# Performance work log

Hardware: AMD Instinct MI355X
Metric: run time of the kernel (lower is better)

## Reference

```python
import jax, jax.numpy as jnp
import numpy as np

RMS_EPS = 1e-8
Q_EPS = 1e-5

def rms_norm(x):
    # RMSNorm without learnable scale, as in BitNet reference BitLinear
    return x * jax.lax.rsqrt(jnp.mean(x * x, axis=-1, keepdims=True) + RMS_EPS)

def activation_quant(x):
    # per-token absmax int8 quant/dequant
    scale = 127.0 / jnp.clip(jnp.max(jnp.abs(x), axis=-1, keepdims=True), Q_EPS)
    return jnp.clip(jnp.round(x * scale), -128, 127) / scale

def weight_quant(w):
    # ternary absmean quant/dequant
    scale = 1.0 / jnp.clip(jnp.mean(jnp.abs(w)), Q_EPS)
    return jnp.clip(jnp.round(w * scale), -1, 1) / scale

def bitlinear(x, w):
    # forward path of BitLinear: RMSNorm -> quantized matmul (STE is identity in fwd)
    xn = rms_norm(x)
    xq = xn + jax.lax.stop_gradient(activation_quant(xn) - xn)
    wq = w + jax.lax.stop_gradient(weight_quant(w) - w)
    return jnp.einsum('bsh,oh->bso', xq, wq)

def setup_inputs() -> dict:
    key = jax.random.key(0)
    k1, k2, k3 = jax.random.split(key, 3)
    H, I = 2048, 8192  # hidden_size, intermediate_size = 4*H
    x = jax.random.normal(k1, (4, 2048, H), jnp.float32)
    w_gate = jax.random.normal(k2, (2 * I, H), jnp.float32) * 0.02
    w_down = jax.random.normal(k3, (H, I), jnp.float32) * 0.02
    return {"x": x, "w_gate": w_gate, "w_down": w_down}

def reference(x, w_gate, w_down):
    y = bitlinear(x, w_gate)          # [B,S,2I]
    gate, v = jnp.split(y, 2, axis=-1)
    return bitlinear(jax.nn.silu(gate) * v, w_down)  # [B,S,H]
```

## Files before the change

kernel.cpp:

```cpp
#include <hip/hip_runtime.h>


using char8  = __attribute__((ext_vector_type(8))) signed char;
using int4v  = __attribute__((ext_vector_type(4))) int;
using half8  = __attribute__((ext_vector_type(8))) _Float16;

__device__ __forceinline__ void glds16(const void* g, void* l) {
  __builtin_amdgcn_global_load_lds((const __attribute__((address_space(1))) void*)g,
                                   (__attribute__((address_space(3))) void*)l, 16, 0, 0);
}

#define SB0() __builtin_amdgcn_sched_barrier(0)

__global__ __launch_bounds__(256) void reduce_abs_kernel(
    const float4* __restrict__ w, float* __restrict__ partials, int n4) {
  int t = threadIdx.x;
  int gid = blockIdx.x * 256 + t;
  int stride = gridDim.x * 256;
  float s = 0.f;
  for (int i = gid; i < n4; i += stride) {
    float4 u = w[i];
    s += fabsf(u.x) + fabsf(u.y) + fabsf(u.z) + fabsf(u.w);
  }
  __shared__ float sm[256];
  sm[t] = s; __syncthreads();
  for (int off = 128; off > 0; off >>= 1) {
    if (t < off) sm[t] += sm[t + off];
    __syncthreads();
  }
  if (t == 0) partials[blockIdx.x] = sm[0];
}

__global__ __launch_bounds__(256) void finalize_kernel(
    const float* __restrict__ pf, float* __restrict__ scales) {
  __shared__ float sm[256];
  int t = threadIdx.x;
  float s = pf[t] + pf[t + 256] + pf[t + 512] + pf[t + 768];
  sm[t] = s; __syncthreads();
  for (int off = 128; off > 0; off >>= 1) {
    if (t < off) sm[t] += sm[t + off];
    __syncthreads();
  }
  if (t == 0) {
    float c = fmaxf(sm[0] / 33554432.0f, 1e-5f);
    scales[0] = c; scales[2] = 1.0f / c;
  }
  __syncthreads();
  s = pf[1024 + t] + pf[1280 + t] + pf[1536 + t] + pf[1792 + t];
  sm[t] = s; __syncthreads();
  for (int off = 128; off > 0; off >>= 1) {
    if (t < off) sm[t] += sm[t + off];
    __syncthreads();
  }
  if (t == 0) {
    float c = fmaxf(sm[0] / 16777216.0f, 1e-5f);
    scales[1] = c; scales[3] = 1.0f / c;
  }
}

__global__ __launch_bounds__(256) void quant_weight_kernel(
    const float4* __restrict__ w, char8* __restrict__ wq,
    const float* __restrict__ invp, int n8) {
  float inv = *invp;
  int stride = gridDim.x * 256;
  for (int i = blockIdx.x * 256 + threadIdx.x; i < n8; i += stride) {
    float4 a = w[2 * i], b = w[2 * i + 1];
    float v[8] = {a.x, a.y, a.z, a.w, b.x, b.y, b.z, b.w};
    char8 o;
#pragma unroll
    for (int j = 0; j < 8; ++j) {
      float q = rintf(v[j] * inv);
      q = fminf(fmaxf(q, -1.f), 1.f);
      o[j] = (signed char)(int)q;
    }
    wq[i] = o;
  }
}

__global__ __launch_bounds__(256) void act_quant_f32_kernel(
    const float* __restrict__ in, signed char* __restrict__ out,
    float* __restrict__ fscale) {
  const int token = blockIdx.x, t = threadIdx.x;
  const float4* row = (const float4*)(in + (size_t)token * 2048);
  float4 a = row[2 * t], b = row[2 * t + 1];
  float v[8] = {a.x, a.y, a.z, a.w, b.x, b.y, b.z, b.w};
  float ss = 0.f, am = 0.f;
#pragma unroll
  for (int j = 0; j < 8; ++j) { ss += v[j] * v[j]; am = fmaxf(am, fabsf(v[j])); }
  __shared__ float s1[256], s2[256];
  s1[t] = ss; s2[t] = am; __syncthreads();
  for (int off = 128; off > 0; off >>= 1) {
    if (t < off) { s1[t] += s1[t + off]; s2[t] = fmaxf(s2[t], s2[t + off]); }
    __syncthreads();
  }
  float r = 1.0f / sqrtf(s1[0] * (1.0f / 2048.0f) + 1e-8f);
  float f = fmaxf(s2[0] * r, 1e-5f);
  float s = 127.0f / f;
  if (t == 0) fscale[token] = f * (1.0f / 127.0f);
  char8 o;
#pragma unroll
  for (int j = 0; j < 8; ++j) {
    float q = rintf((v[j] * r) * s);
    q = fminf(fmaxf(q, -128.f), 127.f);
    o[j] = (signed char)(int)q;
  }
  ((char8*)(out + (size_t)token * 2048))[t] = o;
}

__global__ __launch_bounds__(256) void act_quant_h_kernel(
    const _Float16* __restrict__ in, signed char* __restrict__ out,
    float* __restrict__ fscale) {
  const int token = blockIdx.x, t = threadIdx.x;
  const half8* row = (const half8*)(in + (size_t)token * 8192);
  float v[32];
  float ss = 0.f, am = 0.f;
#pragma unroll
  for (int c = 0; c < 4; ++c) {
    half8 u = row[c * 256 + t];
#pragma unroll
    for (int j = 0; j < 8; ++j) {
      float f = (float)u[j]; v[c * 8 + j] = f;
      ss += f * f; am = fmaxf(am, fabsf(f));
    }
  }
  __shared__ float s1[256], s2[256];
  s1[t] = ss; s2[t] = am; __syncthreads();
  for (int off = 128; off > 0; off >>= 1) {
    if (t < off) { s1[t] += s1[t + off]; s2[t] = fmaxf(s2[t], s2[t + off]); }
    __syncthreads();
  }
  float r = 1.0f / sqrtf(s1[0] * (1.0f / 8192.0f) + 1e-8f);
  float f = fmaxf(s2[0] * r, 1e-5f);
  float s = 127.0f / f;
  if (t == 0) fscale[token] = f * (1.0f / 127.0f);
#pragma unroll
  for (int c = 0; c < 4; ++c) {
    char8 o;
#pragma unroll
    for (int j = 0; j < 8; ++j) {
      float q = rintf((v[c * 8 + j] * r) * s);
      q = fminf(fmaxf(q, -128.f), 127.f);
      o[j] = (signed char)(int)q;
    }
    ((char8*)(out + (size_t)token * 8192))[c * 256 + t] = o;
  }
}

__global__ __launch_bounds__(256, 2) void gemm1_kernel(
    const signed char* __restrict__ A,
    const signed char* __restrict__ B,
    const float* __restrict__ f1, const float* __restrict__ cgp,
    _Float16* __restrict__ Z) {
  constexpr int K = 2048, I = 8192, NT = K / 64;
  constexpr int BUF = 24576;
  __shared__ __align__(16) signed char Ls[3 * BUF];
  const int t0 = blockIdx.y * 128, n0 = blockIdx.x * 128;
  const int tid = threadIdx.x, w = tid >> 6, l = tid & 63;
  const int wm = (w >> 1) * 64, wn = (w & 1) * 64;
  const int lrow = l & 15, lchunk = (l >> 4) * 16;

  int4v ag[4][4], av[4][4];
#pragma unroll
  for (int i = 0; i < 4; ++i)
#pragma unroll
    for (int j = 0; j < 4; ++j) { ag[i][j] = {0,0,0,0}; av[i][j] = {0,0,0,0}; }

  const signed char* src[6];
  int dst[6];
#pragma unroll
  for (int r = 0; r < 6; ++r) {
    int u = w * 6 + r;
    if (u < 8) {
      src[r] = A + (size_t)(t0 + u * 16 + lrow) * K + lchunk;
      dst[r] = u * 1024;
    } else {
      int v = u - 8;
      int grow = (v < 8) ? (n0 + v * 16 + lrow) : (I + n0 + (v - 8) * 16 + lrow);
      src[r] = B + (size_t)grow * K + lchunk;
      dst[r] = 8192 + v * 1024;
    }
  }

#pragma unroll
  for (int p = 0; p < 2; ++p)
#pragma unroll
    for (int r = 0; r < 6; ++r) glds16(src[r] + p * 64, &Ls[p * BUF + dst[r]]);
  asm volatile("s_waitcnt vmcnt(6)" ::: "memory");
  __builtin_amdgcn_s_barrier();
  SB0();

  const int aoff = (wm >> 4) * 1024 + l * 16;
  const int goff = 8192 + (wn >> 4) * 1024 + l * 16;
  const int voff = goff + 8 * 1024;

  int curo = 0;
  for (int it = 0; it < NT; ++it) {
    int stgo = curo + 2 * BUF; if (stgo >= 3 * BUF) stgo -= 3 * BUF;
    const bool stg = (it + 2 < NT);
    const int ko = (it + 2) * 64;
    int4v af[4], bg[4], bv[4];

#pragma unroll
    for (int j = 0; j < 4; ++j) {
      if (j == 0) {
#pragma unroll
        for (int i = 0; i < 4; ++i) af[i] = *(const int4v*)&Ls[curo + aoff + i * 1024];
      }
      bg[j] = *(const int4v*)&Ls[curo + goff + j * 1024];
      bv[j] = *(const int4v*)&Ls[curo + voff + j * 1024];
      if (stg && j < 3) {
        glds16(src[2 * j] + ko, &Ls[stgo + dst[2 * j]]);
        glds16(src[2 * j + 1] + ko, &Ls[stgo + dst[2 * j + 1]]);
      }
      SB0();
      __builtin_amdgcn_s_barrier();
      SB0();
      __builtin_amdgcn_s_setprio(1);
#pragma unroll
      for (int i = 0; i < 4; ++i)
        ag[i][j] = __builtin_amdgcn_mfma_i32_16x16x64_i8(af[i], bg[j], ag[i][j], 0, 0, 0);
#pragma unroll
      for (int i = 0; i < 4; ++i)
        av[i][j] = __builtin_amdgcn_mfma_i32_16x16x64_i8(af[i], bv[j], av[i][j], 0, 0, 0);
      __builtin_amdgcn_s_setprio(0);
      SB0();
      if (j < 3) {
        __builtin_amdgcn_s_barrier();
        SB0();
      }
    }
    if (it < NT - 2)       asm volatile("s_waitcnt vmcnt(6)" ::: "memory");
    else if (it == NT - 2) asm volatile("s_waitcnt vmcnt(0)" ::: "memory");
    if (it + 1 < NT) {
      __builtin_amdgcn_s_barrier();
      SB0();
    }
    curo += BUF; if (curo == 3 * BUF) curo = 0;
  }

  float cg = *cgp;
#pragma unroll
  for (int i = 0; i < 4; ++i)
#pragma unroll
    for (int rr = 0; rr < 4; ++rr) {
      int m = wm + i * 16 + (l >> 4) * 4 + rr;
      float fs = f1[t0 + m] * cg;
#pragma unroll
      for (int j = 0; j < 4; ++j) {
        int n = wn + j * 16 + (l & 15);
        float g = (float)ag[i][j][rr] * fs, vv = (float)av[i][j][rr] * fs;
        float z = g / (1.0f + __expf(-g)) * vv;
        Z[(size_t)(t0 + m) * I + n0 + n] = (_Float16)z;
      }
    }
}

__global__ __launch_bounds__(256, 2) void gemm2_kernel(
    const signed char* __restrict__ A,
    const signed char* __restrict__ B,
    const float* __restrict__ f2, const float* __restrict__ cdp,
    float* __restrict__ out) {
  constexpr int K = 8192, N = 2048, NT = K / 64;
  constexpr int BUF = 24576;
  __shared__ __align__(16) signed char Ls[3 * BUF];
  const int t0 = blockIdx.y * 128, n0 = blockIdx.x * 256;
  const int tid = threadIdx.x, w = tid >> 6, l = tid & 63;
  const int wm = (w >> 1) * 64, wn = (w & 1) * 128;
  const int lrow = l & 15, lchunk = (l >> 4) * 16;

  int4v acc[4][8];
#pragma unroll
  for (int i = 0; i < 4; ++i)
#pragma unroll
    for (int j = 0; j < 8; ++j) acc[i][j] = {0,0,0,0};

  const signed char* src[6];
  int dst[6];
#pragma unroll
  for (int r = 0; r < 6; ++r) {
    int u = w * 6 + r;
    if (u < 8) {
      src[r] = A + (size_t)(t0 + u * 16 + lrow) * K + lchunk;
      dst[r] = u * 1024;
    } else {
      int v = u - 8;
      src[r] = B + (size_t)(n0 + v * 16 + lrow) * K + lchunk;
      dst[r] = 8192 + v * 1024;
    }
  }

#pragma unroll
  for (int p = 0; p < 2; ++p)
#pragma unroll
    for (int r = 0; r < 6; ++r) glds16(src[r] + p * 64, &Ls[p * BUF + dst[r]]);
  asm volatile("s_waitcnt vmcnt(6)" ::: "memory");
  __builtin_amdgcn_s_barrier();
  SB0();

  const int aoff = (wm >> 4) * 1024 + l * 16;
  const int boff = 8192 + (wn >> 4) * 1024 + l * 16;

  int curo = 0;
  for (int it = 0; it < NT; ++it) {
    int stgo = curo + 2 * BUF; if (stgo >= 3 * BUF) stgo -= 3 * BUF;
    const bool stg = (it + 2 < NT);
    const int ko = (it + 2) * 64;
    int4v af[4], bf[8];

#pragma unroll
    for (int p = 0; p < 4; ++p) {
      if (p == 0) {
#pragma unroll
        for (int i = 0; i < 4; ++i) af[i] = *(const int4v*)&Ls[curo + aoff + i * 1024];
      }
      bf[2 * p]     = *(const int4v*)&Ls[curo + boff + (2 * p) * 1024];
      bf[2 * p + 1] = *(const int4v*)&Ls[curo + boff + (2 * p + 1) * 1024];
      if (stg && p < 3) {
        glds16(src[2 * p] + ko, &Ls[stgo + dst[2 * p]]);
        glds16(src[2 * p + 1] + ko, &Ls[stgo + dst[2 * p + 1]]);
      }
      SB0();
      __builtin_amdgcn_s_barrier();
      SB0();
      __builtin_amdgcn_s_setprio(1);
#pragma unroll
      for (int i = 0; i < 4; ++i)
        acc[i][2 * p] = __builtin_amdgcn_mfma_i32_16x16x64_i8(af[i], bf[2 * p], acc[i][2 * p], 0, 0, 0);
#pragma unroll
      for (int i = 0; i < 4; ++i)
        acc[i][2 * p + 1] = __builtin_amdgcn_mfma_i32_16x16x64_i8(af[i], bf[2 * p + 1], acc[i][2 * p + 1], 0, 0, 0);
      __builtin_amdgcn_s_setprio(0);
      SB0();
      if (p < 3) {
        __builtin_amdgcn_s_barrier();
        SB0();
      }
    }
    if (it < NT - 2)       asm volatile("s_waitcnt vmcnt(6)" ::: "memory");
    else if (it == NT - 2) asm volatile("s_waitcnt vmcnt(0)" ::: "memory");
    if (it + 1 < NT) {
      __builtin_amdgcn_s_barrier();
      SB0();
    }
    curo += BUF; if (curo == 3 * BUF) curo = 0;
  }

  float cd = *cdp;
#pragma unroll
  for (int i = 0; i < 4; ++i)
#pragma unroll
    for (int rr = 0; rr < 4; ++rr) {
      int m = wm + i * 16 + (l >> 4) * 4 + rr;
      float fs = f2[t0 + m] * cd;
#pragma unroll
      for (int j = 0; j < 8; ++j) {
        int n = wn + j * 16 + (l & 15);
        out[(size_t)(t0 + m) * N + n0 + n] = (float)acc[i][j][rr] * fs;
      }
    }
}

extern "C" void kernel_launch(void* const* d_in, const int* in_sizes, int n_in,
                              void* d_out, int out_size, void* d_ws, size_t ws_size,
                              hipStream_t stream) {
  const float* x  = (const float*)d_in[0];
  const float* wg = (const float*)d_in[1];
  const float* wd = (const float*)d_in[2];
  float* out = (float*)d_out;

  char* ws = (char*)d_ws;
  signed char* wgq = (signed char*)(ws);
  signed char* wdq = (signed char*)(ws + 33554432);
  signed char* xq  = (signed char*)(ws + 50331648);
  signed char* zq  = (signed char*)(ws + 67108864);
  _Float16*    z   = (_Float16*)  (ws + 134217728);
  float* f1     = (float*)(ws + 268435456);
  float* f2     = (float*)(ws + 268468224);
  float* pf     = (float*)(ws + 268500992);
  float* scales = (float*)(ws + 268509184);

  reduce_abs_kernel<<<1024, 256, 0, stream>>>((const float4*)wg, pf, 8388608);
  reduce_abs_kernel<<<1024, 256, 0, stream>>>((const float4*)wd, pf + 1024, 4194304);
  finalize_kernel<<<1, 256, 0, stream>>>(pf, scales);

  quant_weight_kernel<<<2048, 256, 0, stream>>>((const float4*)wg, (char8*)wgq, scales + 2, 4194304);
  quant_weight_kernel<<<1024, 256, 0, stream>>>((const float4*)wd, (char8*)wdq, scales + 3, 2097152);
  act_quant_f32_kernel<<<8192, 256, 0, stream>>>(x, xq, f1);

  gemm1_kernel<<<dim3(64, 64), 256, 0, stream>>>(xq, wgq, f1, scales, z);

  act_quant_h_kernel<<<8192, 256, 0, stream>>>(z, zq, f2);

  gemm2_kernel<<<dim3(8, 64), 256, 0, stream>>>(zq, wdq, f2, scales + 1, out);
}
```

Before: 902.8 us.

## Double GEMM block tiles to 256 rows with 512-thread blocks

Both int8 GEMM kernels now use 512-thread blocks covering 256 token rows, with 8 waves arranged 2x4 and larger LDS stages. This is meant to increase data reuse per block and cut global/L2 traffic for the A and B operands. The cost is more LDS per block, which likely limits residency to one block per CU, plus a changed wave tile shape and an explicit LDS wait before the MFMAs.

```diff
diff --git a/kernel.cpp b/kernel.cpp
--- a/kernel.cpp
+++ b/kernel.cpp
@@ -146,108 +146,99 @@
   }
 }
 
-__global__ __launch_bounds__(256, 2) void gemm1_kernel(
+__global__ __launch_bounds__(512, 2) void gemm1_kernel(
     const signed char* __restrict__ A,
     const signed char* __restrict__ B,
     const float* __restrict__ f1, const float* __restrict__ cgp,
     _Float16* __restrict__ Z) {
   constexpr int K = 2048, I = 8192, NT = K / 64;
-  constexpr int BUF = 24576;
+  constexpr int ASZ = 16384, BUF = 32768;
   __shared__ __align__(16) signed char Ls[3 * BUF];
-  const int t0 = blockIdx.y * 128, n0 = blockIdx.x * 128;
+  const int t0 = blockIdx.y * 256, n0 = blockIdx.x * 128;
   const int tid = threadIdx.x, w = tid >> 6, l = tid & 63;
-  const int wm = (w >> 1) * 64, wn = (w & 1) * 64;
+  const int wr = w >> 2, wc = w & 3;
   const int lrow = l & 15, lchunk = (l >> 4) * 16;
 
-  int4v ag[4][4], av[4][4];
-#pragma unroll
-  for (int i = 0; i < 4; ++i)
-#pragma unroll
-    for (int j = 0; j < 4; ++j) { ag[i][j] = {0,0,0,0}; av[i][j] = {0,0,0,0}; }
-
-  const signed char* src[6];
-  int dst[6];
-#pragma unroll
-  for (int r = 0; r < 6; ++r) {
-    int u = w * 6 + r;
-    if (u < 8) {
-      src[r] = A + (size_t)(t0 + u * 16 + lrow) * K + lchunk;
-      dst[r] = u * 1024;
-    } else {
-      int v = u - 8;
-      int grow = (v < 8) ? (n0 + v * 16 + lrow) : (I + n0 + (v - 8) * 16 + lrow);
-      src[r] = B + (size_t)grow * K + lchunk;
-      dst[r] = 8192 + v * 1024;
-    }
-  }
+  int4v ag[8][2], av[8][2];
+#pragma unroll
+  for (int i = 0; i < 8; ++i)
+#pragma unroll
+    for (int j = 0; j < 2; ++j) { ag[i][j] = {0,0,0,0}; av[i][j] = {0,0,0,0}; }
+
+  const signed char* src[4];
+  int dst[4];
+  src[0] = A + (size_t)(t0 + w * 16 + lrow) * K + lchunk;       dst[0] = w * 1024;
+  src[1] = A + (size_t)(t0 + (w + 8) * 16 + lrow) * K + lchunk; dst[1] = (w + 8) * 1024;
+  src[2] = B + (size_t)(n0 + w * 16 + lrow) * K + lchunk;       dst[2] = ASZ + w * 1024;
+  src[3] = B + (size_t)(I + n0 + w * 16 + lrow) * K + lchunk;   dst[3] = ASZ + (8 + w) * 1024;
 
 #pragma unroll
   for (int p = 0; p < 2; ++p)
 #pragma unroll
-    for (int r = 0; r < 6; ++r) glds16(src[r] + p * 64, &Ls[p * BUF + dst[r]]);
-  asm volatile("s_waitcnt vmcnt(6)" ::: "memory");
+    for (int r = 0; r < 4; ++r) glds16(src[r] + p * 64, &Ls[p * BUF + dst[r]]);
+  asm volatile("s_waitcnt vmcnt(4)" ::: "memory");
   __builtin_amdgcn_s_barrier();
   SB0();
 
-  const int aoff = (wm >> 4) * 1024 + l * 16;
-  const int goff = 8192 + (wn >> 4) * 1024 + l * 16;
-  const int voff = goff + 8 * 1024;
+  const int abase = (8 * wr) * 1024 + l * 16;
+  const int gbase = ASZ + (2 * wc) * 1024 + l * 16;
+  const int vbase = ASZ + (8 + 2 * wc) * 1024 + l * 16;
 
   int curo = 0;
   for (int it = 0; it < NT; ++it) {
     int stgo = curo + 2 * BUF; if (stgo >= 3 * BUF) stgo -= 3 * BUF;
     const bool stg = (it + 2 < NT);
     const int ko = (it + 2) * 64;
-    int4v af[4], bg[4], bv[4];
-
-#pragma unroll
-    for (int j = 0; j < 4; ++j) {
-      if (j == 0) {
-#pragma unroll
-        for (int i = 0; i < 4; ++i) af[i] = *(const int4v*)&Ls[curo + aoff + i * 1024];
-      }
-      bg[j] = *(const int4v*)&Ls[curo + goff + j * 1024];
-      bv[j] = *(const int4v*)&Ls[curo + voff + j * 1024];
-      if (stg && j < 3) {
-        glds16(src[2 * j] + ko, &Ls[stgo + dst[2 * j]]);
-        glds16(src[2 * j + 1] + ko, &Ls[stgo + dst[2 * j + 1]]);
-      }
+    int4v bg0, bg1, bv0, bv1;
+
+#pragma unroll
+    for (int q = 0; q < 4; ++q) {
+      int4v a0 = *(const int4v*)&Ls[curo + abase + (2 * q) * 1024];
+      int4v a1 = *(const int4v*)&Ls[curo + abase + (2 * q + 1) * 1024];
+      if (q == 0) {
+        bg0 = *(const int4v*)&Ls[curo + gbase];
+        bg1 = *(const int4v*)&Ls[curo + gbase + 1024];
+        bv0 = *(const int4v*)&Ls[curo + vbase];
+        bv1 = *(const int4v*)&Ls[curo + vbase + 1024];
+      }
+      if (stg) glds16(src[q] + ko, &Ls[stgo + dst[q]]);
       SB0();
       __builtin_amdgcn_s_barrier();
+      asm volatile("s_waitcnt lgkmcnt(0)" ::: "memory");
       SB0();
       __builtin_amdgcn_s_setprio(1);
-#pragma unroll
-      for (int i = 0; i < 4; ++i)
-        ag[i][j] = __builtin_amdgcn_mfma_i32_16x16x64_i8(af[i], bg[j], ag[i][j], 0, 0, 0);
-#pragma unroll
-      for (int i = 0; i < 4; ++i)
-        av[i][j] = __builtin_amdgcn_mfma_i32_16x16x64_i8(af[i], bv[j], av[i][j], 0, 0, 0);
+      ag[2*q  ][0] = __builtin_amdgcn_mfma_i32_16x16x64_i8(a0, bg0, ag[2*q  ][0], 0, 0, 0);
+      ag[2*q  ][1] = __builtin_amdgcn_mfma_i32_16x16x64_i8(a0, bg1, ag[2*q  ][1], 0, 0, 0);
+      av[2*q  ][0] = __builtin_amdgcn_mfma_i32_16x16x64_i8(a0, bv0, av[2*q  ][0], 0, 0, 0);
+      av[2*q  ][1] = __builtin_amdgcn_mfma_i32_16x16x64_i8(a0, bv1, av[2*q  ][1], 0, 0, 0);
+      ag[2*q+1][0] = __builtin_amdgcn_mfma_i32_16x16x64_i8(a1, bg0, ag[2*q+1][0], 0, 0, 0);
+      ag[2*q+1][1] = __builtin_amdgcn_mfma_i32_16x16x64_i8(a1, bg1, ag[2*q+1][1], 0, 0, 0);
+      av[2*q+1][0] = __builtin_amdgcn_mfma_i32_16x16x64_i8(a1, bv0, av[2*q+1][0], 0, 0, 0);
+      av[2*q+1][1] = __builtin_amdgcn_mfma_i32_16x16x64_i8(a1, bv1, av[2*q+1][1], 0, 0, 0);
       __builtin_amdgcn_s_setprio(0);
       SB0();
-      if (j < 3) {
+      if (q < 3) {
         __builtin_amdgcn_s_barrier();
         SB0();
       }
     }
-    if (it < NT - 2)       asm volatile("s_waitcnt vmcnt(6)" ::: "memory");
-    else if (it == NT - 2) asm volatile("s_waitcnt vmcnt(0)" ::: "memory");
-    if (it + 1 < NT) {
-      __builtin_amdgcn_s_barrier();
-      SB0();
-    }
+    if (it < NT - 2) asm volatile("s_waitcnt vmcnt(4)" ::: "memory");
+    else             asm volatile("s_waitcnt vmcnt(0)" ::: "memory");
+    __builtin_amdgcn_s_barrier();
+    SB0();
     curo += BUF; if (curo == 3 * BUF) curo = 0;
   }
 
   float cg = *cgp;
 #pragma unroll
-  for (int i = 0; i < 4; ++i)
+  for (int i = 0; i < 8; ++i)
 #pragma unroll
     for (int rr = 0; rr < 4; ++rr) {
-      int m = wm + i * 16 + (l >> 4) * 4 + rr;
+      int m = 128 * wr + i * 16 + (l >> 4) * 4 + rr;
       float fs = f1[t0 + m] * cg;
 #pragma unroll
-      for (int j = 0; j < 4; ++j) {
-        int n = wn + j * 16 + (l & 15);
+      for (int j = 0; j < 2; ++j) {
+        int n = 32 * wc + j * 16 + (l & 15);
         float g = (float)ag[i][j][rr] * fs, vv = (float)av[i][j][rr] * fs;
         float z = g / (1.0f + __expf(-g)) * vv;
         Z[(size_t)(t0 + m) * I + n0 + n] = (_Float16)z;
@@ -255,106 +246,98 @@
     }
 }
 
-__global__ __launch_bounds__(256, 2) void gemm2_kernel(
+__global__ __launch_bounds__(512, 2) void gemm2_kernel(
     const signed char* __restrict__ A,
     const signed char* __restrict__ B,
     const float* __restrict__ f2, const float* __restrict__ cdp,
     float* __restrict__ out) {
   constexpr int K = 8192, N = 2048, NT = K / 64;
-  constexpr int BUF = 24576;
+  constexpr int ASZ = 16384, BUF = 32768;
   __shared__ __align__(16) signed char Ls[3 * BUF];
-  const int t0 = blockIdx.y * 128, n0 = blockIdx.x * 256;
+  const int t0 = blockIdx.y * 256, n0 = blockIdx.x * 256;
   const int tid = threadIdx.x, w = tid >> 6, l = tid & 63;
-  const int wm = (w >> 1) * 64, wn = (w & 1) * 128;
+  const int wr = w >> 2, wc = w & 3;
   const int lrow = l & 15, lchunk = (l >> 4) * 16;
 
-  int4v acc[4][8];
-#pragma unroll
-  for (int i = 0; i < 4; ++i)
-#pragma unroll
-    for (int j = 0; j < 8; ++j) acc[i][j] = {0,0,0,0};
-
-  const signed char* src[6];
-  int dst[6];
-#pragma unroll
-  for (int r = 0; r < 6; ++r) {
-    int u = w * 6 + r;
-    if (u < 8) {
-      src[r] = A + (size_t)(t0 + u * 16 + lrow) * K + lchunk;
-      dst[r] = u * 1024;
-    } else {
-      int v = u - 8;
-      src[r] = B + (size_t)(n0 + v * 16 + lrow) * K + lchunk;
-      dst[r] = 8192 + v * 1024;
-    }
-  }
+  int4v acc[8][4];
+#pragma unroll
+  for (int i = 0; i < 8; ++i)
+#pragma unroll
+    for (int j = 0; j < 4; ++j) acc[i][j] = {0,0,0,0};
+
+  const signed char* src[4];
+  int dst[4];
+  src[0] = A + (size_t)(t0 + w * 16 + lrow) * K + lchunk;       dst[0] = w * 1024;
+  src[1] = A + (size_t)(t0 + (w + 8) * 16 + lrow) * K + lchunk; dst[1] = (w + 8) * 1024;
+  src[2] = B + (size_t)(n0 + w * 16 + lrow) * K + lchunk;       dst[2] = ASZ + w * 1024;
+  src[3] = B + (size_t)(n0 + (w + 8) * 16 + lrow) * K + lchunk; dst[3] = ASZ + (w + 8) * 1024;
 
 #pragma unroll
   for (int p = 0; p < 2; ++p)
 #pragma unroll
-    for (int r = 0; r < 6; ++r) glds16(src[r] + p * 64, &Ls[p * BUF + dst[r]]);
-  asm volatile("s_waitcnt vmcnt(6)" ::: "memory");
+    for (int r = 0; r < 4; ++r) glds16(src[r] + p * 64, &Ls[p * BUF + dst[r]]);
+  asm volatile("s_waitcnt vmcnt(4)" ::: "memory");
   __builtin_amdgcn_s_barrier();
   SB0();
 
-  const int aoff = (wm >> 4) * 1024 + l * 16;
-  const int boff = 8192 + (wn >> 4) * 1024 + l * 16;
+  const int abase = (8 * wr) * 1024 + l * 16;
+  const int bbase = ASZ + (4 * wc) * 1024 + l * 16;
 
   int curo = 0;
   for (int it = 0; it < NT; ++it) {
     int stgo = curo + 2 * BUF; if (stgo >= 3 * BUF) stgo -= 3 * BUF;
     const bool stg = (it + 2 < NT);
     const int ko = (it + 2) * 64;
-    int4v af[4], bf[8];
-
-#pragma unroll
-    for (int p = 0; p < 4; ++p) {
-      if (p == 0) {
-#pragma unroll
-        for (int i = 0; i < 4; ++i) af[i] = *(const int4v*)&Ls[curo + aoff + i * 1024];
-      }
-      bf[2 * p]     = *(const int4v*)&Ls[curo + boff + (2 * p) * 1024];
-      bf[2 * p + 1] = *(const int4v*)&Ls[curo + boff + (2 * p + 1) * 1024];
-      if (stg && p < 3) {
-        glds16(src[2 * p] + ko, &Ls[stgo + dst[2 * p]]);
-        glds16(src[2 * p + 1] + ko, &Ls[stgo + dst[2 * p + 1]]);
-      }
+    int4v bf0, bf1, bf2, bf3;
+
+#pragma unroll
+    for (int q = 0; q < 4; ++q) {
+      int4v a0 = *(const int4v*)&Ls[curo + abase + (2 * q) * 1024];
+      int4v a1 = *(const int4v*)&Ls[curo + abase + (2 * q + 1) * 1024];
+      if (q == 0) {
+        bf0 = *(const int4v*)&Ls[curo + bbase];
+        bf1 = *(const int4v*)&Ls[curo + bbase + 1024];
+        bf2 = *(const int4v*)&Ls[curo + bbase + 2048];
+        bf3 = *(const int4v*)&Ls[curo + bbase + 3072];
+      }
+      if (stg) glds16(src[q] + ko, &Ls[stgo + dst[q]]);
       SB0();
       __builtin_amdgcn_s_barrier();
+      asm volatile("s_waitcnt lgkmcnt(0)" ::: "memory");
       SB0();
       __builtin_amdgcn_s_setprio(1);
-#pragma unroll
-      for (int i = 0; i < 4; ++i)
-        acc[i][2 * p] = __builtin_amdgcn_mfma_i32_16x16x64_i8(af[i], bf[2 * p], acc[i][2 * p], 0, 0, 0);
-#pragma unroll
-      for (int i = 0; i < 4; ++i)
-        acc[i][2 * p + 1] = __builtin_amdgcn_mfma_i32_16x16x64_i8(af[i], bf[2 * p + 1], acc[i][2 * p + 1], 0, 0, 0);
+      acc[2*q  ][0] = __builtin_amdgcn_mfma_i32_16x16x64_i8(a0, bf0, acc[2*q  ][0], 0, 0, 0);
+      acc[2*q  ][1] = __builtin_amdgcn_mfma_i32_16x16x64_i8(a0, bf1, acc[2*q  ][1], 0, 0, 0);
+      acc[2*q  ][2] = __builtin_amdgcn_mfma_i32_16x16x64_i8(a0, bf2, acc[2*q  ][2], 0, 0, 0);
+      acc[2*q  ][3] = __builtin_amdgcn_mfma_i32_16x16x64_i8(a0, bf3, acc[2*q  ][3], 0, 0, 0);
+      acc[2*q+1][0] = __builtin_amdgcn_mfma_i32_16x16x64_i8(a1, bf0, acc[2*q+1][0], 0, 0, 0);
+      acc[2*q+1][1] = __builtin_amdgcn_mfma_i32_16x16x64_i8(a1, bf1, acc[2*q+1][1], 0, 0, 0);
+      acc[2*q+1][2] = __builtin_amdgcn_mfma_i32_16x16x64_i8(a1, bf2, acc[2*q+1][2], 0, 0, 0);
+      acc[2*q+1][3] = __builtin_amdgcn_mfma_i32_16x16x64_i8(a1, bf3, acc[2*q+1][3], 0, 0, 0);
       __builtin_amdgcn_s_setprio(0);
       SB0();
-      if (p < 3) {
+      if (q < 3) {
         __builtin_amdgcn_s_barrier();
         SB0();
       }
     }
-    if (it < NT - 2)       asm volatile("s_waitcnt vmcnt(6)" ::: "memory");
-    else if (it == NT - 2) asm volatile("s_waitcnt vmcnt(0)" ::: "memory");
-    if (it + 1 < NT) {
-      __builtin_amdgcn_s_barrier();
-      SB0();
-    }
+    if (it < NT - 2) asm volatile("s_waitcnt vmcnt(4)" ::: "memory");
+    else             asm volatile("s_waitcnt vmcnt(0)" ::: "memory");
+    __builtin_amdgcn_s_barrier();
+    SB0();
     curo += BUF; if (curo == 3 * BUF) curo = 0;
   }
 
   float cd = *cdp;
 #pragma unroll
-  for (int i = 0; i < 4; ++i)
+  for (int i = 0; i < 8; ++i)
 #pragma unroll
     for (int rr = 0; rr < 4; ++rr) {
-      int m = wm + i * 16 + (l >> 4) * 4 + rr;
+      int m = 128 * wr + i * 16 + (l >> 4) * 4 + rr;
       float fs = f2[t0 + m] * cd;
 #pragma unroll
-      for (int j = 0; j < 8; ++j) {
-        int n = wn + j * 16 + (l & 15);
+      for (int j = 0; j < 4; ++j) {
+        int n = 64 * wc + j * 16 + (l & 15);
         out[(size_t)(t0 + m) * N + n0 + n] = (float)acc[i][j][rr] * fs;
       }
     }
@@ -387,9 +370,9 @@
   quant_weight_kernel<<<1024, 256, 0, stream>>>((const float4*)wd, (char8*)wdq, scales + 3, 2097152);
   act_quant_f32_kernel<<<8192, 256, 0, stream>>>(x, xq, f1);
 
-  gemm1_kernel<<<dim3(64, 64), 256, 0, stream>>>(xq, wgq, f1, scales, z);
+  gemm1_kernel<<<dim3(64, 32), 512, 0, stream>>>(xq, wgq, f1, scales, z);
 
   act_quant_h_kernel<<<8192, 256, 0, stream>>>(z, zq, f2);
 
-  gemm2_kernel<<<dim3(8, 64), 256, 0, stream>>>(zq, wdq, f2, scales + 1, out);
-}
+  gemm2_kernel<<<dim3(8, 32), 512, 0, stream>>>(zq, wdq, f2, scales + 1, out);
+}
```

Result: faster. 804.2 us (-10.9%).
